# Performance work log

Hardware: AMD Instinct MI355X
Metric: run time of the kernel (lower is better)

## Reference

```python
import jax, jax.numpy as jnp
import numpy as np

B, S, D, E, H, K = 2, 2048, 1024, 8, 4096, 2


def setup_inputs() -> dict:
    key = jax.random.key(0)
    ks = jax.random.split(key, 8)
    w = lambda i, shape: jax.random.normal(ks[i], shape, jnp.float32) * 0.02
    return {
        "x": jax.random.normal(ks[0], (B, S, D), jnp.float32),
        "noise": jax.random.normal(ks[1], (B, S, E), jnp.float32),
        "Wg": w(2, (E, D)),
        "noise_weight": jnp.zeros((E,), jnp.float32),
        "W1": w(3, (E, D, H)),
        "b1": jnp.zeros((E, H), jnp.float32),
        "W2": w(4, (E, D, H)),
        "b2": jnp.zeros((E, H), jnp.float32),
        "Wp": w(5, (E, H, D)),
        "bp": jnp.zeros((E, D), jnp.float32),
        "k": K,
    }


def reference(x, noise, Wg, noise_weight, W1, b1, W2, b2, Wp, bp, k):
    Bb, Ss, Dd = x.shape
    Ee = Wg.shape[0]
    # --- noisy top-k gate (noisy_std = 1.0) ---
    logits = jnp.einsum('bsd,ed->bse', x, Wg)
    noisy = logits + noise * noise_weight            # [B,S,E]
    vals, idx = jax.lax.top_k(noisy, k)              # [B,S,k]
    oh = jax.nn.one_hot(idx, Ee, dtype=x.dtype)      # [B,S,k,E]
    sel = oh.sum(axis=-2) > 0                        # [B,S,E] selected mask
    scat = (oh * vals[..., None]).sum(axis=-2)       # scatter topk logits
    sparse = jnp.where(sel, scat, -jnp.inf)
    gate = jax.nn.softmax(sparse, axis=-1)           # zero weight off-topk
    # --- dense-equivalent expert compute (gate==0 off top-k => same math as masked dispatch) ---
    xf = x.reshape(Bb * Ss, Dd)                      # [T,D]
    gf = gate.reshape(Bb * Ss, Ee)                   # [T,E]
    h1 = jnp.einsum('td,edh->eth', xf, W1) + b1[:, None, :]
    h2 = jnp.einsum('td,edh->eth', xf, W2) + b2[:, None, :]
    hh = h1 * jax.nn.silu(h2)                        # SwiGLU
    outs = jnp.einsum('eth,ehd->etd', hh, Wp) + bp[:, None, :]
    final = jnp.einsum('etd,te->td', outs, gf).reshape(Bb, Ss, Dd)
    return final, idx
```

## Files before the change

### kernel.cpp

```cpp
#include <hip/hip_runtime.h>
#include <math.h>

#define Bc 2
#define Sc 2048
#define Dc 1024
#define Ec 8
#define Hc 4096
#define Tc (Bc*Sc)
#define NSLOT (Tc*2)
#define SLOTPAD 8448
#define FINAL_N ((size_t)Tc*Dc)
#define PROWS ((size_t)SLOTPAD*32)

typedef float f32x4 __attribute__((ext_vector_type(4)));
typedef __bf16 bf16x8 __attribute__((ext_vector_type(8)));

__device__ __forceinline__ unsigned short f2bf(float f) {
    union { float f; unsigned int u; } v; v.f = f;
    return (unsigned short)((v.u + 0x7fffu + ((v.u >> 16) & 1u)) >> 16);
}
__device__ __forceinline__ unsigned int pack2bf(float a, float b) {
    return (unsigned int)f2bf(a) | ((unsigned int)f2bf(b) << 16);
}

__device__ __forceinline__ void gload16(const unsigned short* g, unsigned short* l) {
    __builtin_amdgcn_global_load_lds(
        (const __attribute__((address_space(1))) unsigned int*)g,
        (__attribute__((address_space(3))) unsigned int*)l,
        16, 0, 0);
}

__global__ void k_transpose_panel(const float* __restrict__ inA, const float* __restrict__ inB,
                                  unsigned short* __restrict__ outA, unsigned short* __restrict__ outB,
                                  int R, int C, int nz_per_mat) {
    __shared__ float tile[64][65];
    int z = blockIdx.z;
    const float* in; unsigned short* out;
    if (z < nz_per_mat) { in = inA; out = outA; }
    else { in = inB; out = outB; z -= nz_per_mat; }
    size_t zbase = (size_t)z * (size_t)R * C;
    int R32 = R >> 5;
    int cb = blockIdx.x * 64, rb = blockIdx.y * 64;
    int t = threadIdx.x;
    int q = t & 15, g = t >> 4;
    #pragma unroll
    for (int j = 0; j < 4; j++) {
        int row = g + 16*j;
        float4 v = *(const float4*)&in[zbase + (size_t)(rb+row)*C + cb + q*4];
        tile[row][q*4+0] = v.x; tile[row][q*4+1] = v.y;
        tile[row][q*4+2] = v.z; tile[row][q*4+3] = v.w;
    }
    __syncthreads();
    #pragma unroll
    for (int j = 0; j < 4; j++) {
        int co = g + 16*j;
        int c = cb + co;
        int r0 = rb + q*4;
        ushort4 o;
        o.x = f2bf(tile[q*4+0][co]); o.y = f2bf(tile[q*4+1][co]);
        o.z = f2bf(tile[q*4+2][co]); o.w = f2bf(tile[q*4+3][co]);
        int cr = c & 127;
        int ch = ((r0 >> 3) & 3) ^ ((cr >> 1) & 3);
        size_t off = zbase + (((size_t)(c >> 7) * R32 + (r0 >> 5)) * 4096)
                   + (size_t)cr * 32 + ch * 8 + (r0 & 7);
        *(ushort4*)&out[off] = o;
    }
}

__global__ void k_gate(const float* __restrict__ x, const float* __restrict__ noise,
                       const float* __restrict__ Wg, const float* __restrict__ nw,
                       float* __restrict__ out_idx, int* __restrict__ counts,
                       int* __restrict__ tok_top, float* __restrict__ tok_w) {
    int t = blockIdx.x;
    int lane = threadIdx.x;
    const float* xr = x + (size_t)t * Dc;
    double acc[Ec];
    #pragma unroll
    for (int e = 0; e < Ec; e++) acc[e] = 0.0;
    for (int i = 0; i < Dc/64; i++) {
        int d = lane + i*64;
        double xv = (double)xr[d];
        #pragma unroll
        for (int e = 0; e < Ec; e++) acc[e] += xv * (double)Wg[e*Dc + d];
    }
    #pragma unroll
    for (int e = 0; e < Ec; e++)
        for (int off = 32; off > 0; off >>= 1)
            acc[e] += __shfl_down(acc[e], off);
    if (lane == 0) {
        double noisy[Ec];
        #pragma unroll
        for (int e = 0; e < Ec; e++)
            noisy[e] = acc[e] + (double)noise[t*Ec + e] * (double)nw[e];
        int i0 = 0;
        for (int e = 1; e < Ec; e++) if (noisy[e] > noisy[i0]) i0 = e;
        int i1 = -1;
        for (int e = 0; e < Ec; e++) {
            if (e == i0) continue;
            if (i1 < 0 || noisy[e] > noisy[i1]) i1 = e;
        }
        double ee = exp(noisy[i1] - noisy[i0]);
        float w0 = (float)(1.0 / (1.0 + ee));
        float w1 = (float)(ee / (1.0 + ee));
        out_idx[t*2 + 0] = (float)i0;
        out_idx[t*2 + 1] = (float)i1;
        tok_top[t*2] = i0; tok_top[t*2+1] = i1;
        tok_w[t*2] = w0;   tok_w[t*2+1] = w1;
        atomicAdd(&counts[i0], 1);
        atomicAdd(&counts[i1], 1);
    }
}

__global__ void k_scan(const int* __restrict__ counts, int* __restrict__ offsets) {
    if (threadIdx.x == 0) {
        int s = 0;
        for (int e = 0; e < Ec; e++) { offsets[e] = s; s += counts[e]; }
        offsets[Ec] = s;
    }
}

__global__ void k_fill(const int* __restrict__ tok_top, const int* __restrict__ offsets,
                       int* __restrict__ fill, int* __restrict__ slot_token,
                       int* __restrict__ slot_of, int* __restrict__ slot_pos) {
    int t = blockIdx.x * 256 + threadIdx.x;
    if (t >= Tc) return;
    #pragma unroll
    for (int j = 0; j < 2; j++) {
        int e = tok_top[t*2 + j];
        int pos = atomicAdd(&fill[e], 1);
        int slot = offsets[e] + pos;
        slot_token[slot] = t;
        slot_of[t*2 + j] = slot;
        slot_pos[slot] = pos;
    }
}

__global__ void k_packA(const float* __restrict__ x, const int* __restrict__ slot_token,
                        const int* __restrict__ slot_pos, unsigned short* __restrict__ apk) {
    int s = blockIdx.x * 4 + (threadIdx.x >> 6);
    int lane = threadIdx.x & 63;
    int token = slot_token[s];
    int pos = slot_pos[s];
    const float4* px = (const float4*)(x + (size_t)token * Dc) + lane*4;
    float4 v0 = px[0], v1 = px[1], v2 = px[2], v3 = px[3];
    uint4 lo, hi;
    lo.x = pack2bf(v0.x, v0.y); lo.y = pack2bf(v0.z, v0.w);
    lo.z = pack2bf(v1.x, v1.y); lo.w = pack2bf(v1.z, v1.w);
    hi.x = pack2bf(v2.x, v2.y); hi.y = pack2bf(v2.z, v2.w);
    hi.z = pack2bf(v3.x, v3.y); hi.w = pack2bf(v3.z, v3.w);
    int kp = lane >> 1;
    int key = (pos >> 1) & 3;
    int c0 = (lane & 1) * 2;
    size_t base = (size_t)kp * PROWS + (size_t)s * 32;
    *(uint4*)&apk[base + ((c0 ^ key) * 8)]       = lo;
    *(uint4*)&apk[base + (((c0+1) ^ key) * 8)]   = hi;
}

__global__ __launch_bounds__(256, 4) void k_gemm1(
    const unsigned short* __restrict__ apk,
    const unsigned short* __restrict__ w1p, const unsigned short* __restrict__ w2p,
    const float* __restrict__ b1, const float* __restrict__ b2,
    const int* __restrict__ counts, const int* __restrict__ offsets,
    unsigned short* __restrict__ hh2) {
    int e = blockIdx.z;
    int n_e = counts[e];
    int m0 = blockIdx.y * 128;
    if (m0 >= n_e) return;
    int base = offsets[e];
    int bx = blockIdx.x;
    int n0 = bx * 64;
    int hp = bx >> 1, ro = (bx & 1) * 64;

    __shared__ __align__(16) unsigned char smem[32768];
    unsigned short* sA = (unsigned short*)smem;
    unsigned short* sB = (unsigned short*)(smem + 16384);
    float* sS = (float*)smem;

    int tid = threadIdx.x;
    int wid = tid >> 6, lane = tid & 63;
    int wr = wid >> 1, wc = wid & 1;

    const unsigned short* aSrc = apk + (size_t)(base + m0 + wid*32)*32 + lane*8;
    const unsigned short* wmat = (wid < 2) ? w1p : w2p;
    const unsigned short* bSrc = wmat + ((size_t)(e*32 + hp) * 32) * 4096
                               + (size_t)(ro + (wid & 1)*32)*32 + lane*8;

    int arow = lane & 15, cr = lane >> 4;
    int ccf = cr ^ ((arow >> 1) & 3);
    int aoff[4], boff[4];
    #pragma unroll
    for (int m = 0; m < 4; m++) aoff[m] = (wr*64 + m*16 + arow)*32 + ccf*8;
    #pragma unroll
    for (int n = 0; n < 4; n++) boff[n] = (wc*64 + n*16 + arow)*32 + ccf*8;

    f32x4 acc[4][4];
    #pragma unroll
    for (int m = 0; m < 4; m++)
        #pragma unroll
        for (int n = 0; n < 4; n++)
            #pragma unroll
            for (int j = 0; j < 4; j++) acc[m][n][j] = 0.0f;

    unsigned short* dA = sA + wid*1024;
    unsigned short* dB = sB + wid*1024;

    const int NK = Dc / 32;
    for (int kk = 0; kk < NK; ++kk) {
        const unsigned short* a = aSrc + (size_t)kk*PROWS;
        const unsigned short* b = bSrc + (size_t)kk*4096;
        gload16(a,       dA); gload16(a + 512, dA + 512);
        gload16(b,       dB); gload16(b + 512, dB + 512);
        __syncthreads();
        bf16x8 af[4], bf[4];
        #pragma unroll
        for (int m = 0; m < 4; m++) af[m] = *(const bf16x8*)&sA[aoff[m]];
        #pragma unroll
        for (int n = 0; n < 4; n++) bf[n] = *(const bf16x8*)&sB[boff[n]];
        #pragma unroll
        for (int m = 0; m < 4; m++)
            #pragma unroll
            for (int n = 0; n < 4; n++)
                acc[m][n] = __builtin_amdgcn_mfma_f32_16x16x32_bf16(af[m], bf[n], acc[m][n], 0, 0, 0);
        __syncthreads();
    }

    int lrow = (lane >> 4) * 4, lcol = lane & 15;
    if (wc == 1) {
        #pragma unroll
        for (int n = 0; n < 4; n++) {
            float b2v = b2[e*Hc + n0 + n*16 + lcol];
            #pragma unroll
            for (int m = 0; m < 4; m++) {
                int rb = wr*64 + m*16 + lrow;
                #pragma unroll
                for (int j = 0; j < 4; j++) {
                    float h2 = acc[m][n][j] + b2v;
                    sS[(rb + j)*64 + n*16 + lcol] = h2 / (1.0f + expf(-h2));
                }
            }
        }
    }
    __syncthreads();
    if (wc == 0) {
        #pragma unroll
        for (int n = 0; n < 4; n++) {
            int hcol = n0 + n*16 + lcol;
            float b1v = b1[e*Hc + hcol];
            int hp2 = hcol >> 5;
            int ch  = (hcol >> 3) & 3;
            int ho  = hcol & 7;
            #pragma unroll
            for (int m = 0; m < 4; m++) {
                int rb = wr*64 + m*16 + lrow;
                #pragma unroll
                for (int j = 0; j < 4; j++) {
                    int r = m0 + rb + j;
                    if (r < n_e) {
                        float v = (acc[m][n][j] + b1v) * sS[(rb + j)*64 + n*16 + lcol];
                        int key = (r >> 1) & 3;
                        hh2[(size_t)hp2 * PROWS + (size_t)(base + r)*32 + ((ch ^ key)*8) + ho] = f2bf(v);
                    }
                }
            }
        }
    }
}

__global__ __launch_bounds__(256, 4) void k_gemm2(
    const unsigned short* __restrict__ hh2,
    const unsigned short* __restrict__ wpp,
    const float* __restrict__ bp,
    const int* __restrict__ counts, const int* __restrict__ offsets,
    float* __restrict__ outb) {
    int e = blockIdx.z;
    int n_e = counts[e];
    int m0 = blockIdx.y * 128;
    if (m0 >= n_e) return;
    int base = offsets[e];
    int dp = blockIdx.x;
    int n0 = dp * 128;

    __shared__ __align__(16) unsigned short sA[128*32];
    __shared__ __align__(16) unsigned short sB[128*32];

    int tid = threadIdx.x;
    int wid = tid >> 6, lane = tid & 63;
    int wr = wid >> 1, wc = wid & 1;

    const unsigned short* aSrc = hh2 + (size_t)(base + m0 + wid*32)*32 + lane*8;
    const unsigned short* bSrc = wpp + ((size_t)(e*8 + dp) * 128) * 4096
                               + wid*1024 + lane*8;

    int arow = lane & 15, cr = lane >> 4;
    int ccf = cr ^ ((arow >> 1) & 3);
    int aoff[4], boff[4];
    #pragma unroll
    for (int m = 0; m < 4; m++) aoff[m] = (wr*64 + m*16 + arow)*32 + ccf*8;
    #pragma unroll
    for (int n = 0; n < 4; n++) boff[n] = (wc*64 + n*16 + arow)*32 + ccf*8;

    f32x4 acc[4][4];
    #pragma unroll
    for (int m = 0; m < 4; m++)
        #pragma unroll
        for (int n = 0; n < 4; n++)
            #pragma unroll
            for (int j = 0; j < 4; j++) acc[m][n][j] = 0.0f;

    unsigned short* dA = sA + wid*1024;
    unsigned short* dB = sB + wid*1024;

    const int NK = Hc / 32;
    for (int kk = 0; kk < NK; ++kk) {
        const unsigned short* a = aSrc + (size_t)kk*PROWS;
        const unsigned short* b = bSrc + (size_t)kk*4096;
        gload16(a,       dA); gload16(a + 512, dA + 512);
        gload16(b,       dB); gload16(b + 512, dB + 512);
        __syncthreads();
        bf16x8 af[4], bf[4];
        #pragma unroll
        for (int m = 0; m < 4; m++) af[m] = *(const bf16x8*)&sA[aoff[m]];
        #pragma unroll
        for (int n = 0; n < 4; n++) bf[n] = *(const bf16x8*)&sB[boff[n]];
        #pragma unroll
        for (int m = 0; m < 4; m++)
            #pragma unroll
            for (int n = 0; n < 4; n++)
                acc[m][n] = __builtin_amdgcn_mfma_f32_16x16x32_bf16(af[m], bf[n], acc[m][n], 0, 0, 0);
        __syncthreads();
    }

    int lrow = (lane >> 4) * 4, lcol = lane & 15;
    #pragma unroll
    for (int n = 0; n < 4; n++) {
        int dcol = n0 + wc*64 + n*16 + lcol;
        float bias = bp[e*Dc + dcol];
        #pragma unroll
        for (int m = 0; m < 4; m++) {
            int rb2 = m0 + wr*64 + m*16 + lrow;
            #pragma unroll
            for (int j = 0; j < 4; j++) {
                int r = rb2 + j;
                if (r < n_e)
                    outb[(size_t)(base + r)*Dc + dcol] = acc[m][n][j] + bias;
            }
        }
    }
}

__global__ void k_combine(const float* __restrict__ outb, const int* __restrict__ slot_of,
                          const float* __restrict__ tok_w, float* __restrict__ final_out) {
    int gid = blockIdx.x * 256 + threadIdx.x;
    int t = gid >> 8;
    int c = (gid & 255) * 4;
    int s0 = slot_of[t*2], s1 = slot_of[t*2 + 1];
    float w0 = tok_w[t*2], w1 = tok_w[t*2 + 1];
    float4 o0 = *(const float4*)&outb[(size_t)s0*Dc + c];
    float4 o1 = *(const float4*)&outb[(size_t)s1*Dc + c];
    float4 r;
    r.x = w0*o0.x + w1*o1.x;
    r.y = w0*o0.y + w1*o1.y;
    r.z = w0*o0.z + w1*o1.z;
    r.w = w0*o0.w + w1*o1.w;
    *(float4*)&final_out[(size_t)t*Dc + c] = r;
}

extern "C" void kernel_launch(void* const* d_in, const int* in_sizes, int n_in,
                              void* d_out, int out_size, void* d_ws, size_t ws_size,
                              hipStream_t stream) {
    (void)in_sizes; (void)n_in; (void)out_size; (void)ws_size;
    const float* x     = (const float*)d_in[0];
    const float* noise = (const float*)d_in[1];
    const float* Wg    = (const float*)d_in[2];
    const float* nw    = (const float*)d_in[3];
    const float* W1    = (const float*)d_in[4];
    const float* b1    = (const float*)d_in[5];
    const float* W2    = (const float*)d_in[6];
    const float* b2    = (const float*)d_in[7];
    const float* Wp    = (const float*)d_in[8];
    const float* bp    = (const float*)d_in[9];

    char* ws = (char*)d_ws;
    size_t off = 0;
    unsigned short* W1P = (unsigned short*)(ws + off); off += (size_t)Ec*Dc*Hc*2;
    unsigned short* W2P = (unsigned short*)(ws + off); off += (size_t)Ec*Dc*Hc*2;
    unsigned short* WPP = (unsigned short*)(ws + off); off += (size_t)Ec*Hc*Dc*2;
    unsigned short* APK = (unsigned short*)(ws + off); off += (size_t)32*PROWS*2;
    unsigned short* HH2 = (unsigned short*)(ws + off); off += (size_t)128*PROWS*2;
    float*          OUTB= (float*)(ws + off);          off += (size_t)NSLOT*Dc*4;
    int*   counts    = (int*)(ws + off);
    int*   fill      = (int*)(ws + off + 32);
    int*   offsets   = (int*)(ws + off + 64);
    int*   tok_top   = (int*)(ws + off + 128);
    float* tok_w     = (float*)(ws + off + 128 + (size_t)Tc*2*4);
    int*   slot_token= (int*)(ws + off + 128 + (size_t)Tc*2*8);
    int*   slot_of   = (int*)(ws + off + 128 + (size_t)Tc*2*8 + (size_t)NSLOT*4);
    int*   slot_pos  = (int*)(ws + off + 128 + (size_t)Tc*2*8 + (size_t)NSLOT*8);

    float* final_out = (float*)d_out;
    float* idx_out   = (float*)d_out + FINAL_N;

    hipMemsetAsync(counts, 0, 64, stream);

    k_transpose_panel<<<dim3(Hc/64, Dc/64, 2*Ec), 256, 0, stream>>>(W1, W2, W1P, W2P, Dc, Hc, Ec);
    k_transpose_panel<<<dim3(Dc/64, Hc/64, Ec), 256, 0, stream>>>(Wp, Wp, WPP, WPP, Hc, Dc, Ec);

    k_gate<<<Tc, 64, 0, stream>>>(x, noise, Wg, nw, idx_out, counts, tok_top, tok_w);
    k_scan<<<1, 64, 0, stream>>>(counts, offsets);
    k_fill<<<Tc/256, 256, 0, stream>>>(tok_top, offsets, fill, slot_token, slot_of, slot_pos);
    k_packA<<<NSLOT/4, 256, 0, stream>>>(x, slot_token, slot_pos, APK);

    k_gemm1<<<dim3(Hc/64, Tc/128, Ec), 256, 0, stream>>>(APK, W1P, W2P, b1, b2,
                                                         counts, offsets, HH2);
    k_gemm2<<<dim3(Dc/128, Tc/128, Ec), 256, 0, stream>>>(HH2, WPP, bp, counts, offsets, OUTB);
    k_combine<<<(Tc*Dc/4)/256, 256, 0, stream>>>(OUTB, slot_of, tok_w, final_out);
}
```

Before: 660.0 us.

## Double-buffer LDS tiles in both expert GEMMs with async prefetch two stages ahead

```diff
diff --git a/kernel.cpp b/kernel.cpp
--- a/kernel.cpp
+++ b/kernel.cpp
@@ -28,6 +28,12 @@
         (const __attribute__((address_space(1))) unsigned int*)g,
         (__attribute__((address_space(3))) unsigned int*)l,
         16, 0, 0);
+}
+
+__device__ __forceinline__ void fence_bar() {
+    __builtin_amdgcn_sched_barrier(0);
+    asm volatile("s_barrier" ::: "memory");
+    __builtin_amdgcn_sched_barrier(0);
 }
 
 __global__ void k_transpose_panel(const float* __restrict__ inA, const float* __restrict__ inB,
@@ -172,8 +178,7 @@
     int hp = bx >> 1, ro = (bx & 1) * 64;
 
     __shared__ __align__(16) unsigned char smem[32768];
-    unsigned short* sA = (unsigned short*)smem;
-    unsigned short* sB = (unsigned short*)(smem + 16384);
+    unsigned short* sU = (unsigned short*)smem;
     float* sS = (float*)smem;
 
     int tid = threadIdx.x;
@@ -191,7 +196,7 @@
     #pragma unroll
     for (int m = 0; m < 4; m++) aoff[m] = (wr*64 + m*16 + arow)*32 + ccf*8;
     #pragma unroll
-    for (int n = 0; n < 4; n++) boff[n] = (wc*64 + n*16 + arow)*32 + ccf*8;
+    for (int n = 0; n < 4; n++) boff[n] = 8192 + (wc*64 + n*16 + arow)*32 + ccf*8;
 
     f32x4 acc[4][4];
     #pragma unroll
@@ -201,27 +206,35 @@
             #pragma unroll
             for (int j = 0; j < 4; j++) acc[m][n][j] = 0.0f;
 
-    unsigned short* dA = sA + wid*1024;
-    unsigned short* dB = sB + wid*1024;
-
-    const int NK = Dc / 32;
-    for (int kk = 0; kk < NK; ++kk) {
+    auto STAGE = [&](int s, int kk) {
         const unsigned short* a = aSrc + (size_t)kk*PROWS;
         const unsigned short* b = bSrc + (size_t)kk*4096;
+        unsigned short* dA = sU + s*4096 + wid*1024;
+        unsigned short* dB = sU + 8192 + s*4096 + wid*1024;
         gload16(a,       dA); gload16(a + 512, dA + 512);
         gload16(b,       dB); gload16(b + 512, dB + 512);
-        __syncthreads();
+    };
+
+    const int NK = Dc / 32;
+    STAGE(0, 0); STAGE(1, 1);
+    for (int kk = 0; kk < NK; ++kk) {
+        int s = kk & 1;
+        const unsigned short* sl = sU + s*4096;
+        if (kk < NK - 1) { asm volatile("s_waitcnt vmcnt(4)" ::: "memory"); }
+        else             { asm volatile("s_waitcnt vmcnt(0)" ::: "memory"); }
+        fence_bar();
         bf16x8 af[4], bf[4];
         #pragma unroll
-        for (int m = 0; m < 4; m++) af[m] = *(const bf16x8*)&sA[aoff[m]];
-        #pragma unroll
-        for (int n = 0; n < 4; n++) bf[n] = *(const bf16x8*)&sB[boff[n]];
+        for (int m = 0; m < 4; m++) af[m] = *(const bf16x8*)&sl[aoff[m]];
+        #pragma unroll
+        for (int n = 0; n < 4; n++) bf[n] = *(const bf16x8*)&sl[boff[n]];
         #pragma unroll
         for (int m = 0; m < 4; m++)
             #pragma unroll
             for (int n = 0; n < 4; n++)
                 acc[m][n] = __builtin_amdgcn_mfma_f32_16x16x32_bf16(af[m], bf[n], acc[m][n], 0, 0, 0);
-        __syncthreads();
+        fence_bar();
+        if (kk + 2 < NK) STAGE(s, kk + 2);
     }
 
     int lrow = (lane >> 4) * 4, lcol = lane & 15;
@@ -235,7 +248,7 @@
                 #pragma unroll
                 for (int j = 0; j < 4; j++) {
                     float h2 = acc[m][n][j] + b2v;
-                    sS[(rb + j)*64 + n*16 + lcol] = h2 / (1.0f + expf(-h2));
+                    sS[(rb + j)*64 + ((n*16 + lcol) ^ (j << 4))] = h2 / (1.0f + expf(-h2));
                 }
             }
         }
@@ -256,7 +269,7 @@
                 for (int j = 0; j < 4; j++) {
                     int r = m0 + rb + j;
                     if (r < n_e) {
-                        float v = (acc[m][n][j] + b1v) * sS[(rb + j)*64 + n*16 + lcol];
+                        float v = (acc[m][n][j] + b1v) * sS[(rb + j)*64 + ((n*16 + lcol) ^ (j << 4))];
                         int key = (r >> 1) & 3;
                         hh2[(size_t)hp2 * PROWS + (size_t)(base + r)*32 + ((ch ^ key)*8) + ho] = f2bf(v);
                     }
@@ -280,8 +293,8 @@
     int dp = blockIdx.x;
     int n0 = dp * 128;
 
-    __shared__ __align__(16) unsigned short sA[128*32];
-    __shared__ __align__(16) unsigned short sB[128*32];
+    __shared__ __align__(16) unsigned char smem[32768];
+    unsigned short* sU = (unsigned short*)smem;
 
     int tid = threadIdx.x;
     int wid = tid >> 6, lane = tid & 63;
@@ -297,7 +310,7 @@
     #pragma unroll
     for (int m = 0; m < 4; m++) aoff[m] = (wr*64 + m*16 + arow)*32 + ccf*8;
     #pragma unroll
-    for (int n = 0; n < 4; n++) boff[n] = (wc*64 + n*16 + arow)*32 + ccf*8;
+    for (int n = 0; n < 4; n++) boff[n] = 8192 + (wc*64 + n*16 + arow)*32 + ccf*8;
 
     f32x4 acc[4][4];
     #pragma unroll
@@ -307,27 +320,35 @@
             #pragma unroll
             for (int j = 0; j < 4; j++) acc[m][n][j] = 0.0f;
 
-    unsigned short* dA = sA + wid*1024;
-    unsigned short* dB = sB + wid*1024;
-
-    const int NK = Hc / 32;
-    for (int kk = 0; kk < NK; ++kk) {
+    auto STAGE = [&](int s, int kk) {
         const unsigned short* a = aSrc + (size_t)kk*PROWS;
         const unsigned short* b = bSrc + (size_t)kk*4096;
+        unsigned short* dA = sU + s*4096 + wid*1024;
+        unsigned short* dB = sU + 8192 + s*4096 + wid*1024;
         gload16(a,       dA); gload16(a + 512, dA + 512);
         gload16(b,       dB); gload16(b + 512, dB + 512);
-        __syncthreads();
+    };
+
+    const int NK = Hc / 32;
+    STAGE(0, 0); STAGE(1, 1);
+    for (int kk = 0; kk < NK; ++kk) {
+        int s = kk & 1;
+        const unsigned short* sl = sU + s*4096;
+        if (kk < NK - 1) { asm volatile("s_waitcnt vmcnt(4)" ::: "memory"); }
+        else             { asm volatile("s_waitcnt vmcnt(0)" ::: "memory"); }
+        fence_bar();
         bf16x8 af[4], bf[4];
         #pragma unroll
-        for (int m = 0; m < 4; m++) af[m] = *(const bf16x8*)&sA[aoff[m]];
-        #pragma unroll
-        for (int n = 0; n < 4; n++) bf[n] = *(const bf16x8*)&sB[boff[n]];
+        for (int m = 0; m < 4; m++) af[m] = *(const bf16x8*)&sl[aoff[m]];
+        #pragma unroll
+        for (int n = 0; n < 4; n++) bf[n] = *(const bf16x8*)&sl[boff[n]];
         #pragma unroll
         for (int m = 0; m < 4; m++)
             #pragma unroll
             for (int n = 0; n < 4; n++)
                 acc[m][n] = __builtin_amdgcn_mfma_f32_16x16x32_bf16(af[m], bf[n], acc[m][n], 0, 0, 0);
-        __syncthreads();
+        fence_bar();
+        if (kk + 2 < NK) STAGE(s, kk + 2);
     }
 
     int lrow = (lane >> 4) * 4, lcol = lane & 15;
@@ -400,7 +421,7 @@
     float* final_out = (float*)d_out;
     float* idx_out   = (float*)d_out + FINAL_N;
 
-    hipMemsetAsync(counts, 0, 64, stream);
+    (void)hipMemsetAsync(counts, 0, 64, stream);
 
     k_transpose_panel<<<dim3(Hc/64, Dc/64, 2*Ec), 256, 0, stream>>>(W1, W2, W1P, W2P, Dc, Hc, Ec);
     k_transpose_panel<<<dim3(Dc/64, Hc/64, Ec), 256, 0, stream>>>(Wp, Wp, WPP, WPP, Hc, Dc, Ec);
```

After: 645.9 us. 2.1% less time.
